# Kernel tuning notes

Hardware: AMD Instinct MI355X
Metric: run time of the kernel (lower is better)

The kernel has to match this reference:

```python
import jax, jax.numpy as jnp
import numpy as np

C = 768
HEADS = 12

def setup_inputs() -> dict:
    key = jax.random.key(0)
    k1, k2, k3 = jax.random.split(key, 3)
    x = jax.random.normal(k1, (8, C, 32, 32), dtype=jnp.float32)
    # 1x1 convs are channel-wise linear maps; store as [out_c, in_c]
    w_qkv = jax.random.normal(k2, (3 * C, C), dtype=jnp.float32) * (C ** -0.5)
    w_proj = jax.random.normal(k3, (C, C), dtype=jnp.float32) * (C ** -0.5)
    return {"x": x, "w_qkv": w_qkv, "w_proj": w_proj}

def reference(x, w_qkv, w_proj):
    b, c, h, w = x.shape
    heads = HEADS
    dh = c // heads
    n = h * w
    scale = dh ** -0.5
    # 1x1 conv QKV: [b, 3c, h, w] -> [b, 3, heads, dh, n]
    qkv = jnp.einsum('oc,bchw->bohw', w_qkv, x).reshape(b, 3, heads, dh, n)
    q, k, v = qkv[:, 0], qkv[:, 1], qkv[:, 2]  # each [b, heads, dh, n]
    attn = jnp.einsum('bhdn,bhdm->bhnm', q, k) * scale  # [b, heads, n, n]
    attn = jax.nn.softmax(attn, axis=-1)
    out = jnp.einsum('bhnm,bhdm->bhdn', attn, v)  # [b, heads, dh, n]
    out = out.reshape(b, c, h, w)
    return jnp.einsum('oc,bchw->bohw', w_proj, out)
```

## Files before the change

### kernel.cpp

```cpp
#include <hip/hip_runtime.h>

typedef unsigned short u16;
typedef unsigned int u32;
typedef float v4f __attribute__((ext_vector_type(4)));
typedef __bf16 bf16x8 __attribute__((ext_vector_type(8)));

#define BATCH 8
#define CDIM 768
#define NHEAD 12
#define DH 64
#define NSEQ 1024
#define SCL 0.18033688011112042f

__device__ __forceinline__ u16 f2bf(float f) {
  u32 u = __builtin_bit_cast(u32, f);
  u += 0x7fffu + ((u >> 16) & 1u);
  return (u16)(u >> 16);
}

__device__ __forceinline__ u16 b16(float f) {
  return (u16)((__builtin_bit_cast(u32, f) + 0x8000u) >> 16);
}

__device__ __forceinline__ u32 pkbf(float hi, float lo) {
  u32 a = __builtin_bit_cast(u32, hi) + 0x8000u;
  u32 b = __builtin_bit_cast(u32, lo) + 0x8000u;
  return __builtin_amdgcn_perm(a, b, 0x07060302u);
}

__device__ __forceinline__ v4f mfma16(bf16x8 a, bf16x8 b, v4f c) {
  return __builtin_amdgcn_mfma_f32_16x16x32_bf16(a, b, c, 0, 0, 0);
}

__device__ __forceinline__ void gload16(const u16* g, u16* l) {
  __builtin_amdgcn_global_load_lds(
      (const __attribute__((address_space(1))) void*)g,
      (__attribute__((address_space(3))) void*)l, 16, 0, 0);
}

__global__ __launch_bounds__(256) void k_prep(const float* __restrict__ x,
                                              const float* __restrict__ wq,
                                              const float* __restrict__ wp,
                                              u16* __restrict__ xT,
                                              u16* __restrict__ wqb,
                                              u16* __restrict__ wpb) {
  __shared__ u16 Ts[64][72];
  int bid = blockIdx.x;
  int t = threadIdx.x;
  if (bid < 2304) {
    bool isQ = bid < 1728;
    const float* s = isQ ? wq : wp;
    u16* d = isQ ? wqb : wpb;
    int i = (isQ ? bid : bid - 1728) * 256 + t;
    float4 v = ((const float4*)s)[i];
    u32 lo = (u32)f2bf(v.x) | ((u32)f2bf(v.y) << 16);
    u32 hi = (u32)f2bf(v.z) | ((u32)f2bf(v.w) << 16);
    ((uint2*)d)[i] = uint2{lo, hi};
    return;
  }
  int id = bid - 2304;
  int p0 = (id & 15) * 64; id >>= 4;
  int c0 = (id % 12) * 64; int b = id / 12;
  int cr = t >> 4;
  int p4 = (t & 15) * 4;
  const float* src = x + ((size_t)b * CDIM + c0) * NSEQ + p0;
#pragma unroll
  for (int i = 0; i < 4; ++i) {
    int c = cr + i * 16;
    float4 v = *(const float4*)&src[(size_t)c * NSEQ + p4];
    Ts[p4 + 0][c] = f2bf(v.x);
    Ts[p4 + 1][c] = f2bf(v.y);
    Ts[p4 + 2][c] = f2bf(v.z);
    Ts[p4 + 3][c] = f2bf(v.w);
  }
  __syncthreads();
  int p = t >> 2;
  int cq = t & 3;
  u16* dst = xT + ((size_t)b * NSEQ + p0 + p) * CDIM + c0;
#pragma unroll
  for (int j = 0; j < 2; ++j) {
    int ch = cq + j * 4;
    *(int4*)&dst[ch * 8] = *(const int4*)&Ts[p][ch * 8];
  }
}

#define NKT 12

__device__ __forceinline__ void gemm_core(const u16* __restrict__ Ag,
                                          const u16* __restrict__ Bg,
                                          u16* sm, v4f (&acc)[4][4]) {
  int t = threadIdx.x, lane = t & 63, wid = t >> 6;
  int ln = lane & 15, quad = lane >> 4;
  int wm = wid >> 2, wn = wid & 3;

  int sr = t >> 3;
  int sc = ((t & 7) ^ (sr & 7)) * 8;
  const u16* As0 = Ag + (size_t)sr * CDIM + sc;
  const u16* Bs0 = Bg + (size_t)sr * CDIM + sc;
  int ldw = wid * 512;

  int x = ln & 7;
  int rA = (wm * 64 + ln) * 64;
  int rB = 8192 + (wn * 64 + ln) * 64;
  int c0 = (quad ^ x) * 8;
  int c1 = ((4 + quad) ^ x) * 8;

  {
    u16* sb = sm;
    gload16(As0, sb + ldw);
    gload16(As0 + (size_t)64 * CDIM, sb + 4096 + ldw);
    gload16(Bs0, sb + 8192 + ldw);
    gload16(Bs0 + (size_t)64 * CDIM, sb + 12288 + ldw);
    gload16(Bs0 + (size_t)128 * CDIM, sb + 16384 + ldw);
    gload16(Bs0 + (size_t)192 * CDIM, sb + 20480 + ldw);
  }
  asm volatile("" ::: "memory");
  {
    u16* sb = sm + 24576;
    const u16* Ak = As0 + 64;
    const u16* Bk = Bs0 + 64;
    gload16(Ak, sb + ldw);
    gload16(Ak + (size_t)64 * CDIM, sb + 4096 + ldw);
    gload16(Bk, sb + 8192 + ldw);
    gload16(Bk + (size_t)64 * CDIM, sb + 12288 + ldw);
    gload16(Bk + (size_t)128 * CDIM, sb + 16384 + ldw);
    gload16(Bk + (size_t)192 * CDIM, sb + 20480 + ldw);
  }
  asm volatile("s_waitcnt vmcnt(6)" ::: "memory");
  asm volatile("s_barrier" ::: "memory");

#pragma unroll
  for (int kt = 0; kt < NKT; ++kt) {
    const u16* sb = sm + (kt % 3) * 24576;
    u16* nb = sm + ((kt + 2) % 3) * 24576;
    const u16* Ak = As0 + (kt + 2) * 64;
    const u16* Bk = Bs0 + (kt + 2) * 64;

    bf16x8 af[2][2], bfr[4][2];
#pragma unroll
    for (int m = 0; m < 2; ++m) {
      af[m][0] = *(const bf16x8*)&sb[rA + m * 1024 + c0];
      af[m][1] = *(const bf16x8*)&sb[rA + m * 1024 + c1];
    }
#pragma unroll
    for (int n = 0; n < 4; ++n) {
      bfr[n][0] = *(const bf16x8*)&sb[rB + n * 1024 + c0];
      bfr[n][1] = *(const bf16x8*)&sb[rB + n * 1024 + c1];
    }
    if (kt < NKT - 2) {
      gload16(Ak, nb + ldw);
      gload16(Ak + (size_t)64 * CDIM, nb + 4096 + ldw);
      gload16(Bk, nb + 8192 + ldw);
    }
    asm volatile("s_barrier" ::: "memory");
    asm volatile("s_waitcnt lgkmcnt(0)" ::: "memory");
    __builtin_amdgcn_sched_barrier(0);
    __builtin_amdgcn_s_setprio(1);
#pragma unroll
    for (int m = 0; m < 2; ++m)
#pragma unroll
      for (int n = 0; n < 4; ++n) {
        acc[m][n] = mfma16(af[m][0], bfr[n][0], acc[m][n]);
        acc[m][n] = mfma16(af[m][1], bfr[n][1], acc[m][n]);
      }
    __builtin_amdgcn_s_setprio(0);
    asm volatile("s_barrier" ::: "memory");

#pragma unroll
    for (int m = 0; m < 2; ++m) {
      af[m][0] = *(const bf16x8*)&sb[rA + (m + 2) * 1024 + c0];
      af[m][1] = *(const bf16x8*)&sb[rA + (m + 2) * 1024 + c1];
    }
    if (kt < NKT - 2) {
      gload16(Bk + (size_t)64 * CDIM, nb + 12288 + ldw);
      gload16(Bk + (size_t)128 * CDIM, nb + 16384 + ldw);
      gload16(Bk + (size_t)192 * CDIM, nb + 20480 + ldw);
      asm volatile("s_waitcnt vmcnt(6)" ::: "memory");
    } else if (kt == NKT - 2) {
      asm volatile("s_waitcnt vmcnt(0)" ::: "memory");
    }
    asm volatile("s_barrier" ::: "memory");
    asm volatile("s_waitcnt lgkmcnt(0)" ::: "memory");
    __builtin_amdgcn_sched_barrier(0);
    __builtin_amdgcn_s_setprio(1);
#pragma unroll
    for (int m = 0; m < 2; ++m)
#pragma unroll
      for (int n = 0; n < 4; ++n) {
        acc[m + 2][n] = mfma16(af[m][0], bfr[n][0], acc[m + 2][n]);
        acc[m + 2][n] = mfma16(af[m][1], bfr[n][1], acc[m + 2][n]);
      }
    __builtin_amdgcn_s_setprio(0);
    asm volatile("s_barrier" ::: "memory");
  }
}

__global__ __launch_bounds__(512, 2) void k_gemm_qkv(const u16* __restrict__ Wb,
                                                     const u16* __restrict__ xT,
                                                     u16* __restrict__ qkT,
                                                     u16* __restrict__ vbuf) {
  __shared__ u16 sm[3 * 24576];
  int bid = blockIdx.x;
  int swz = (bid & 7) * 72 + (bid >> 3);
  int oIdx = swz % 18, pIdx = swz / 18;
  int oT = oIdx * 128;
  int pG = pIdx * 256;

  v4f acc[4][4] = {};
  gemm_core(Wb + (size_t)oT * CDIM, xT + (size_t)pG * CDIM, sm, acc);

  int t = threadIdx.x, lane = t & 63, wid = t >> 6;
  int ln = lane & 15, quad = lane >> 4;
  int wm = wid >> 2, wn = wid & 3;
  bool isV = oT >= 2 * CDIM;
#pragma unroll
  for (int m = 0; m < 4; ++m) {
#pragma unroll
    for (int n = 0; n < 4; ++n) {
      int ro = oT + wm * 64 + m * 16 + quad * 4;
      int cp = pG + wn * 64 + n * 16 + ln;
      int b = cp >> 10, p = cp & 1023;
      if (!isV) {
        u32 lo = (u32)f2bf(acc[m][n][0]) | ((u32)f2bf(acc[m][n][1]) << 16);
        u32 hi = (u32)f2bf(acc[m][n][2]) | ((u32)f2bf(acc[m][n][3]) << 16);
        *(uint2*)&qkT[((size_t)b * NSEQ + p) * 1536 + ro] = uint2{lo, hi};
      } else {
#pragma unroll
        for (int r = 0; r < 4; ++r)
          vbuf[((size_t)b * CDIM + (ro - 2 * CDIM + r)) * NSEQ + p] =
              f2bf(acc[m][n][r]);
      }
    }
  }
}

__global__ __launch_bounds__(256) void k_attn(const u16* __restrict__ qkT,
                                              const u16* __restrict__ vbuf,
                                              u16* __restrict__ attnT) {
  int id = blockIdx.x;
  int b = id & 7;
  int j = id >> 3;
  int h = j % 12;
  int nt0 = (j / 12) * 128;

  int t = threadIdx.x, lane = t & 63, wid = t >> 6;
  int ln = lane & 15, quad = lane >> 4;
  int nbase = nt0 + wid * 32;

  __shared__ u16 Ks[2][2][64 * 32];
  __shared__ u16 Vs[2][2][64 * 32];
  __shared__ u16 Pa[4][32 * 72];
  u16* myP = Pa[wid];

  const u16* qbase = qkT + ((size_t)b * NSEQ + nbase) * 1536 + h * DH;
  bf16x8 aq[2][2];
#pragma unroll
  for (int mt = 0; mt < 2; ++mt)
#pragma unroll
    for (int ks = 0; ks < 2; ++ks)
      aq[mt][ks] = *(const bf16x8*)&qbase[(size_t)(mt * 16 + ln) * 1536 + ks * 32 + quad * 8];

  bf16x8 ones;
#pragma unroll
  for (int i = 0; i < 8; ++i) ones[i] = __builtin_bit_cast(__bf16, (u16)0x3F80);

  v4f oacc[2][4] = {};
  v4f lacc[2] = {};

  int lr = lane >> 2, lc = (lane & 3) * 8;
  const u16* kgw = qkT + (size_t)b * NSEQ * 1536 + CDIM + h * DH +
                   (size_t)(wid * 16 + lr) * 1536 + lc;
  const u16* vgw = vbuf + ((size_t)b * CDIM + h * DH + wid * 16 + lr) * NSEQ + lc;
  int sb = (wid * 16) * 32;

  gload16(kgw, &Ks[0][0][sb]);
  gload16(kgw + 32, &Ks[0][1][sb]);
  gload16(vgw, &Vs[0][0][sb]);
  gload16(vgw + 32, &Vs[0][1][sb]);
  __syncthreads();

  for (int s = 0; s < 16; ++s) {
    int cur = s & 1, nxt = cur ^ 1;
    if (s < 15) {
      size_t ko = (size_t)(s + 1) * 64 * 1536;
      int vo = (s + 1) * 64;
      gload16(kgw + ko, &Ks[nxt][0][sb]);
      gload16(kgw + ko + 32, &Ks[nxt][1][sb]);
      gload16(vgw + vo, &Vs[nxt][0][sb]);
      gload16(vgw + vo + 32, &Vs[nxt][1][sb]);
    }

#pragma unroll
    for (int ct = 0; ct < 4; ++ct) {
      bf16x8 kf0 = *(const bf16x8*)&Ks[cur][0][(ct * 16 + ln) * 32 + quad * 8];
      bf16x8 kf1 = *(const bf16x8*)&Ks[cur][1][(ct * 16 + ln) * 32 + quad * 8];
#pragma unroll
      for (int mt = 0; mt < 2; ++mt) {
        v4f sc = {};
        sc = mfma16(kf0, aq[mt][0], sc);
        sc = mfma16(kf1, aq[mt][1], sc);
        float p0 = __builtin_amdgcn_exp2f(sc[0] * SCL);
        float p1 = __builtin_amdgcn_exp2f(sc[1] * SCL);
        float p2 = __builtin_amdgcn_exp2f(sc[2] * SCL);
        float p3 = __builtin_amdgcn_exp2f(sc[3] * SCL);
        *(uint2*)&myP[(mt * 16 + ln) * 72 + ct * 16 + quad * 4] =
            uint2{pkbf(p1, p0), pkbf(p3, p2)};
      }
    }

    bf16x8 ap[2][2];
#pragma unroll
    for (int mt = 0; mt < 2; ++mt)
#pragma unroll
      for (int ks = 0; ks < 2; ++ks)
        ap[mt][ks] = *(const bf16x8*)&myP[(mt * 16 + ln) * 72 + ks * 32 + quad * 8];
#pragma unroll
    for (int mt = 0; mt < 2; ++mt) {
      lacc[mt] = mfma16(ap[mt][0], ones, lacc[mt]);
      lacc[mt] = mfma16(ap[mt][1], ones, lacc[mt]);
    }
#pragma unroll
    for (int nt = 0; nt < 4; ++nt) {
      bf16x8 vf0 = *(const bf16x8*)&Vs[cur][0][(nt * 16 + ln) * 32 + quad * 8];
      bf16x8 vf1 = *(const bf16x8*)&Vs[cur][1][(nt * 16 + ln) * 32 + quad * 8];
#pragma unroll
      for (int mt = 0; mt < 2; ++mt) {
        oacc[mt][nt] = mfma16(ap[mt][0], vf0, oacc[mt][nt]);
        oacc[mt][nt] = mfma16(ap[mt][1], vf1, oacc[mt][nt]);
      }
    }
    __syncthreads();
  }

#pragma unroll
  for (int mt = 0; mt < 2; ++mt) {
#pragma unroll
    for (int r = 0; r < 4; ++r) {
      float inv = 1.0f / lacc[mt][r];
      int n = nbase + mt * 16 + quad * 4 + r;
      u16* dst = attnT + ((size_t)b * NSEQ + n) * CDIM + h * DH;
#pragma unroll
      for (int nt = 0; nt < 4; ++nt)
        dst[nt * 16 + ln] = b16(oacc[mt][nt][r] * inv);
    }
  }
}

__global__ __launch_bounds__(512, 2) void k_gemm_proj(const u16* __restrict__ Wb,
                                                      const u16* __restrict__ aT,
                                                      float* __restrict__ out) {
  __shared__ u16 sm[3 * 24576];
  int bid = blockIdx.x;
  int swz = (bid & 7) * 24 + (bid >> 3);
  int oIdx = swz % 6, pIdx = swz / 6;
  int oT = oIdx * 128;
  int pG = pIdx * 256;

  v4f acc[4][4] = {};
  gemm_core(Wb + (size_t)oT * CDIM, aT + (size_t)pG * CDIM, sm, acc);

  int t = threadIdx.x, lane = t & 63, wid = t >> 6;
  int ln = lane & 15, quad = lane >> 4;
  int wm = wid >> 2, wn = wid & 3;
#pragma unroll
  for (int m = 0; m < 4; ++m) {
#pragma unroll
    for (int n = 0; n < 4; ++n) {
      int ro = oT + wm * 64 + m * 16 + quad * 4;
      int cp = pG + wn * 64 + n * 16 + ln;
      int b = cp >> 10, p = cp & 1023;
#pragma unroll
      for (int r = 0; r < 4; ++r)
        out[((size_t)b * CDIM + ro + r) * NSEQ + p] = acc[m][n][r];
    }
  }
}

extern "C" void kernel_launch(void* const* d_in, const int* in_sizes, int n_in,
                              void* d_out, int out_size, void* d_ws, size_t ws_size,
                              hipStream_t stream) {
  const float* x = (const float*)d_in[0];
  const float* w_qkv = (const float*)d_in[1];
  const float* w_proj = (const float*)d_in[2];
  float* out = (float*)d_out;

  char* ws = (char*)d_ws;
  u16* wqkv_bf = (u16*)(ws);
  u16* wproj_bf = (u16*)(ws + 3538944);
  u16* xT = (u16*)(ws + 4718592);
  u16* vbuf = (u16*)(ws + 17301504);
  u16* qkT = (u16*)d_out;
  u16* attnT = xT;

  k_prep<<<dim3(3840), dim3(256), 0, stream>>>(x, w_qkv, w_proj, xT, wqkv_bf, wproj_bf);
  k_gemm_qkv<<<dim3(576), dim3(512), 0, stream>>>(wqkv_bf, xT, qkT, vbuf);
  k_attn<<<dim3(768), dim3(256), 0, stream>>>(qkT, vbuf, attnT);
  k_gemm_proj<<<dim3(192), dim3(512), 0, stream>>>(wproj_bf, attnT, out);
}
```

Measured before the change: 190.8 us.

## Retile GEMMs to 256x128 with 4 waves and k=32 steps; swizzle attention K/V LDS

The shared GEMM core moves from 8 waves with a 128x256 tile and K-step 64 to 4 waves with a 256x128 tile, K-step 32, and a 3-stage ring unrolled by three. Each wave now holds 8x4 accumulators and a new XOR swizzle for LDS. The aim is more MFMA work per wave and less LDS traffic per FLOP, at the cost of more register pressure and twice as many barriers per K. The attention kernel separately switches its K/V tiles to 64-wide rows with an XOR swizzle to cut LDS bank conflicts.

After: 184.6 us. -3.3%, faster.

```diff
diff --git a/kernel.cpp b/kernel.cpp
--- a/kernel.cpp
+++ b/kernel.cpp
@@ -84,140 +84,128 @@
   }
 }
 
-#define NKT 12
+#define NKT 24
 
 __device__ __forceinline__ void gemm_core(const u16* __restrict__ Ag,
                                           const u16* __restrict__ Bg,
-                                          u16* sm, v4f (&acc)[4][4]) {
+                                          u16* sm, v4f (&acc)[8][4]) {
   int t = threadIdx.x, lane = t & 63, wid = t >> 6;
   int ln = lane & 15, quad = lane >> 4;
-  int wm = wid >> 2, wn = wid & 3;
-
-  int sr = t >> 3;
-  int sc = ((t & 7) ^ (sr & 7)) * 8;
-  const u16* As0 = Ag + (size_t)sr * CDIM + sc;
-  const u16* Bs0 = Bg + (size_t)sr * CDIM + sc;
+  int wm = wid >> 1, wn = wid & 1;
+
+  int srow = wid * 16 + (lane >> 2);
+  int scg = ((lane & 3) ^ ((lane >> 3) & 3)) * 8;
+  const u16* As0 = Ag + (size_t)srow * CDIM + scg;
+  const u16* Bs0 = Bg + (size_t)srow * CDIM + scg;
   int ldw = wid * 512;
 
-  int x = ln & 7;
-  int rA = (wm * 64 + ln) * 64;
-  int rB = 8192 + (wn * 64 + ln) * 64;
-  int c0 = (quad ^ x) * 8;
-  int c1 = ((4 + quad) ^ x) * 8;
+  int cA = (quad ^ ((ln >> 1) & 3)) * 8;
+  int rA = (wm * 128 + ln) * 32;
+  int rB = 8192 + (wn * 64 + ln) * 32;
 
   {
-    u16* sb = sm;
-    gload16(As0, sb + ldw);
-    gload16(As0 + (size_t)64 * CDIM, sb + 4096 + ldw);
-    gload16(Bs0, sb + 8192 + ldw);
-    gload16(Bs0 + (size_t)64 * CDIM, sb + 12288 + ldw);
-    gload16(Bs0 + (size_t)128 * CDIM, sb + 16384 + ldw);
-    gload16(Bs0 + (size_t)192 * CDIM, sb + 20480 + ldw);
+    u16* sb0 = sm;
+    gload16(As0, sb0 + ldw);
+    gload16(As0 + (size_t)64 * CDIM, sb0 + 2048 + ldw);
+    gload16(As0 + (size_t)128 * CDIM, sb0 + 4096 + ldw);
+    gload16(As0 + (size_t)192 * CDIM, sb0 + 6144 + ldw);
+    gload16(Bs0, sb0 + 8192 + ldw);
+    gload16(Bs0 + (size_t)64 * CDIM, sb0 + 10240 + ldw);
   }
   asm volatile("" ::: "memory");
   {
-    u16* sb = sm + 24576;
-    const u16* Ak = As0 + 64;
-    const u16* Bk = Bs0 + 64;
-    gload16(Ak, sb + ldw);
-    gload16(Ak + (size_t)64 * CDIM, sb + 4096 + ldw);
-    gload16(Bk, sb + 8192 + ldw);
-    gload16(Bk + (size_t)64 * CDIM, sb + 12288 + ldw);
-    gload16(Bk + (size_t)128 * CDIM, sb + 16384 + ldw);
-    gload16(Bk + (size_t)192 * CDIM, sb + 20480 + ldw);
+    u16* sb1 = sm + 12288;
+    gload16(As0 + 32, sb1 + ldw);
+    gload16(As0 + (size_t)64 * CDIM + 32, sb1 + 2048 + ldw);
+    gload16(As0 + (size_t)128 * CDIM + 32, sb1 + 4096 + ldw);
+    gload16(As0 + (size_t)192 * CDIM + 32, sb1 + 6144 + ldw);
+    gload16(Bs0 + 32, sb1 + 8192 + ldw);
+    gload16(Bs0 + (size_t)64 * CDIM + 32, sb1 + 10240 + ldw);
   }
   asm volatile("s_waitcnt vmcnt(6)" ::: "memory");
   asm volatile("s_barrier" ::: "memory");
 
-#pragma unroll
-  for (int kt = 0; kt < NKT; ++kt) {
-    const u16* sb = sm + (kt % 3) * 24576;
-    u16* nb = sm + ((kt + 2) % 3) * 24576;
-    const u16* Ak = As0 + (kt + 2) * 64;
-    const u16* Bk = Bs0 + (kt + 2) * 64;
-
-    bf16x8 af[2][2], bfr[4][2];
-#pragma unroll
-    for (int m = 0; m < 2; ++m) {
-      af[m][0] = *(const bf16x8*)&sb[rA + m * 1024 + c0];
-      af[m][1] = *(const bf16x8*)&sb[rA + m * 1024 + c1];
-    }
-#pragma unroll
-    for (int n = 0; n < 4; ++n) {
-      bfr[n][0] = *(const bf16x8*)&sb[rB + n * 1024 + c0];
-      bfr[n][1] = *(const bf16x8*)&sb[rB + n * 1024 + c1];
-    }
-    if (kt < NKT - 2) {
-      gload16(Ak, nb + ldw);
-      gload16(Ak + (size_t)64 * CDIM, nb + 4096 + ldw);
-      gload16(Bk, nb + 8192 + ldw);
-    }
-    asm volatile("s_barrier" ::: "memory");
-    asm volatile("s_waitcnt lgkmcnt(0)" ::: "memory");
-    __builtin_amdgcn_sched_barrier(0);
-    __builtin_amdgcn_s_setprio(1);
-#pragma unroll
-    for (int m = 0; m < 2; ++m)
-#pragma unroll
-      for (int n = 0; n < 4; ++n) {
-        acc[m][n] = mfma16(af[m][0], bfr[n][0], acc[m][n]);
-        acc[m][n] = mfma16(af[m][1], bfr[n][1], acc[m][n]);
-      }
-    __builtin_amdgcn_s_setprio(0);
-    asm volatile("s_barrier" ::: "memory");
-
-#pragma unroll
-    for (int m = 0; m < 2; ++m) {
-      af[m][0] = *(const bf16x8*)&sb[rA + (m + 2) * 1024 + c0];
-      af[m][1] = *(const bf16x8*)&sb[rA + (m + 2) * 1024 + c1];
-    }
-    if (kt < NKT - 2) {
-      gload16(Bk + (size_t)64 * CDIM, nb + 12288 + ldw);
-      gload16(Bk + (size_t)128 * CDIM, nb + 16384 + ldw);
-      gload16(Bk + (size_t)192 * CDIM, nb + 20480 + ldw);
-      asm volatile("s_waitcnt vmcnt(6)" ::: "memory");
-    } else if (kt == NKT - 2) {
-      asm volatile("s_waitcnt vmcnt(0)" ::: "memory");
-    }
-    asm volatile("s_barrier" ::: "memory");
-    asm volatile("s_waitcnt lgkmcnt(0)" ::: "memory");
-    __builtin_amdgcn_sched_barrier(0);
-    __builtin_amdgcn_s_setprio(1);
-#pragma unroll
-    for (int m = 0; m < 2; ++m)
-#pragma unroll
-      for (int n = 0; n < 4; ++n) {
-        acc[m + 2][n] = mfma16(af[m][0], bfr[n][0], acc[m + 2][n]);
-        acc[m + 2][n] = mfma16(af[m][1], bfr[n][1], acc[m + 2][n]);
-      }
-    __builtin_amdgcn_s_setprio(0);
-    asm volatile("s_barrier" ::: "memory");
-  }
-}
-
-__global__ __launch_bounds__(512, 2) void k_gemm_qkv(const u16* __restrict__ Wb,
+  for (int kb = 0; kb < 8; ++kb) {
+#pragma unroll
+    for (int u = 0; u < 3; ++u) {
+      int kt = kb * 3 + u;
+      const u16* sb = sm + u * 12288;
+      u16* nb = sm + ((u + 2) % 3) * 12288;
+      int ko = (kt + 2) * 32;
+
+      bf16x8 af[4], bfr[4];
+#pragma unroll
+      for (int m = 0; m < 4; ++m)
+        af[m] = *(const bf16x8*)&sb[rA + m * 512 + cA];
+#pragma unroll
+      for (int n = 0; n < 4; ++n)
+        bfr[n] = *(const bf16x8*)&sb[rB + n * 512 + cA];
+      if (kt < NKT - 2) {
+        gload16(As0 + ko, nb + ldw);
+        gload16(As0 + (size_t)64 * CDIM + ko, nb + 2048 + ldw);
+        gload16(Bs0 + ko, nb + 8192 + ldw);
+      }
+      asm volatile("s_barrier" ::: "memory");
+      asm volatile("s_waitcnt lgkmcnt(0)" ::: "memory");
+      __builtin_amdgcn_sched_barrier(0);
+      __builtin_amdgcn_s_setprio(1);
+#pragma unroll
+      for (int m = 0; m < 4; ++m)
+#pragma unroll
+        for (int n = 0; n < 4; ++n)
+          acc[m][n] = mfma16(af[m], bfr[n], acc[m][n]);
+      __builtin_amdgcn_s_setprio(0);
+      asm volatile("s_barrier" ::: "memory");
+
+#pragma unroll
+      for (int m = 0; m < 4; ++m)
+        af[m] = *(const bf16x8*)&sb[rA + (m + 4) * 512 + cA];
+      if (kt < NKT - 2) {
+        gload16(As0 + (size_t)128 * CDIM + ko, nb + 4096 + ldw);
+        gload16(As0 + (size_t)192 * CDIM + ko, nb + 6144 + ldw);
+        gload16(Bs0 + (size_t)64 * CDIM + ko, nb + 10240 + ldw);
+        asm volatile("s_waitcnt vmcnt(6)" ::: "memory");
+      } else if (kt == NKT - 2) {
+        asm volatile("s_waitcnt vmcnt(0)" ::: "memory");
+      }
+      asm volatile("s_barrier" ::: "memory");
+      asm volatile("s_waitcnt lgkmcnt(0)" ::: "memory");
+      __builtin_amdgcn_sched_barrier(0);
+      __builtin_amdgcn_s_setprio(1);
+#pragma unroll
+      for (int m = 0; m < 4; ++m)
+#pragma unroll
+        for (int n = 0; n < 4; ++n)
+          acc[m + 4][n] = mfma16(af[m], bfr[n], acc[m + 4][n]);
+      __builtin_amdgcn_s_setprio(0);
+      asm volatile("s_barrier" ::: "memory");
+    }
+  }
+}
+
+__global__ __launch_bounds__(256, 2) void k_gemm_qkv(const u16* __restrict__ Wb,
                                                      const u16* __restrict__ xT,
                                                      u16* __restrict__ qkT,
                                                      u16* __restrict__ vbuf) {
-  __shared__ u16 sm[3 * 24576];
+  __shared__ u16 sm[3 * 12288];
   int bid = blockIdx.x;
   int swz = (bid & 7) * 72 + (bid >> 3);
-  int oIdx = swz % 18, pIdx = swz / 18;
-  int oT = oIdx * 128;
-  int pG = pIdx * 256;
-
-  v4f acc[4][4] = {};
+  int oIdx = swz % 9, pIdx = swz / 9;
+  int oT = oIdx * 256;
+  int pG = pIdx * 128;
+
+  v4f acc[8][4] = {};
   gemm_core(Wb + (size_t)oT * CDIM, xT + (size_t)pG * CDIM, sm, acc);
 
   int t = threadIdx.x, lane = t & 63, wid = t >> 6;
   int ln = lane & 15, quad = lane >> 4;
-  int wm = wid >> 2, wn = wid & 3;
+  int wm = wid >> 1, wn = wid & 1;
   bool isV = oT >= 2 * CDIM;
 #pragma unroll
-  for (int m = 0; m < 4; ++m) {
+  for (int m = 0; m < 8; ++m) {
 #pragma unroll
     for (int n = 0; n < 4; ++n) {
-      int ro = oT + wm * 64 + m * 16 + quad * 4;
+      int ro = oT + wm * 128 + m * 16 + quad * 4;
       int cp = pG + wn * 64 + n * 16 + ln;
       int b = cp >> 10, p = cp & 1023;
       if (!isV) {
@@ -247,8 +235,8 @@
   int ln = lane & 15, quad = lane >> 4;
   int nbase = nt0 + wid * 32;
 
-  __shared__ u16 Ks[2][2][64 * 32];
-  __shared__ u16 Vs[2][2][64 * 32];
+  __shared__ u16 Ks[2][64 * 64];
+  __shared__ u16 Vs[2][64 * 64];
   __shared__ u16 Pa[4][32 * 72];
   u16* myP = Pa[wid];
 
@@ -267,16 +255,19 @@
   v4f oacc[2][4] = {};
   v4f lacc[2] = {};
 
-  int lr = lane >> 2, lc = (lane & 3) * 8;
-  const u16* kgw = qkT + (size_t)b * NSEQ * 1536 + CDIM + h * DH +
-                   (size_t)(wid * 16 + lr) * 1536 + lc;
-  const u16* vgw = vbuf + ((size_t)b * CDIM + h * DH + wid * 16 + lr) * NSEQ + lc;
-  int sb = (wid * 16) * 32;
-
-  gload16(kgw, &Ks[0][0][sb]);
-  gload16(kgw + 32, &Ks[0][1][sb]);
-  gload16(vgw, &Vs[0][0][sb]);
-  gload16(vgw + 32, &Vs[0][1][sb]);
+  int sr8 = lane >> 3;
+  int sch = ((lane & 7) ^ sr8) * 8;
+  const u16* kg0 = qkT + ((size_t)b * NSEQ + wid * 16 + sr8) * 1536 + CDIM + h * DH + sch;
+  const u16* vg0 = vbuf + ((size_t)b * CDIM + h * DH + wid * 16 + sr8) * NSEQ + sch;
+  int sK = (wid * 16) * 64;
+
+  int sw0 = (quad ^ (ln & 7)) * 8;
+  int sw1 = ((4 + quad) ^ (ln & 7)) * 8;
+
+  gload16(kg0, &Ks[0][sK]);
+  gload16(kg0 + (size_t)8 * 1536, &Ks[0][sK + 512]);
+  gload16(vg0, &Vs[0][sK]);
+  gload16(vg0 + 8 * NSEQ, &Vs[0][sK + 512]);
   __syncthreads();
 
   for (int s = 0; s < 16; ++s) {
@@ -284,16 +275,16 @@
     if (s < 15) {
       size_t ko = (size_t)(s + 1) * 64 * 1536;
       int vo = (s + 1) * 64;
-      gload16(kgw + ko, &Ks[nxt][0][sb]);
-      gload16(kgw + ko + 32, &Ks[nxt][1][sb]);
-      gload16(vgw + vo, &Vs[nxt][0][sb]);
-      gload16(vgw + vo + 32, &Vs[nxt][1][sb]);
+      gload16(kg0 + ko, &Ks[nxt][sK]);
+      gload16(kg0 + ko + (size_t)8 * 1536, &Ks[nxt][sK + 512]);
+      gload16(vg0 + vo, &Vs[nxt][sK]);
+      gload16(vg0 + vo + 8 * NSEQ, &Vs[nxt][sK + 512]);
     }
 
 #pragma unroll
     for (int ct = 0; ct < 4; ++ct) {
-      bf16x8 kf0 = *(const bf16x8*)&Ks[cur][0][(ct * 16 + ln) * 32 + quad * 8];
-      bf16x8 kf1 = *(const bf16x8*)&Ks[cur][1][(ct * 16 + ln) * 32 + quad * 8];
+      bf16x8 kf0 = *(const bf16x8*)&Ks[cur][(ct * 16 + ln) * 64 + sw0];
+      bf16x8 kf1 = *(const bf16x8*)&Ks[cur][(ct * 16 + ln) * 64 + sw1];
 #pragma unroll
       for (int mt = 0; mt < 2; ++mt) {
         v4f sc = {};
@@ -321,8 +312,8 @@
     }
 #pragma unroll
     for (int nt = 0; nt < 4; ++nt) {
-      bf16x8 vf0 = *(const bf16x8*)&Vs[cur][0][(nt * 16 + ln) * 32 + quad * 8];
-      bf16x8 vf1 = *(const bf16x8*)&Vs[cur][1][(nt * 16 + ln) * 32 + quad * 8];
+      bf16x8 vf0 = *(const bf16x8*)&Vs[cur][(nt * 16 + ln) * 64 + sw0];
+      bf16x8 vf1 = *(const bf16x8*)&Vs[cur][(nt * 16 + ln) * 64 + sw1];
 #pragma unroll
       for (int mt = 0; mt < 2; ++mt) {
         oacc[mt][nt] = mfma16(ap[mt][0], vf0, oacc[mt][nt]);
@@ -346,27 +337,27 @@
   }
 }
 
-__global__ __launch_bounds__(512, 2) void k_gemm_proj(const u16* __restrict__ Wb,
+__global__ __launch_bounds__(256, 2) void k_gemm_proj(const u16* __restrict__ Wb,
                                                       const u16* __restrict__ aT,
                                                       float* __restrict__ out) {
-  __shared__ u16 sm[3 * 24576];
+  __shared__ u16 sm[3 * 12288];
   int bid = blockIdx.x;
   int swz = (bid & 7) * 24 + (bid >> 3);
-  int oIdx = swz % 6, pIdx = swz / 6;
-  int oT = oIdx * 128;
-  int pG = pIdx * 256;
-
-  v4f acc[4][4] = {};
+  int oIdx = swz % 3, pIdx = swz / 3;
+  int oT = oIdx * 256;
+  int pG = pIdx * 128;
+
+  v4f acc[8][4] = {};
   gemm_core(Wb + (size_t)oT * CDIM, aT + (size_t)pG * CDIM, sm, acc);
 
   int t = threadIdx.x, lane = t & 63, wid = t >> 6;
   int ln = lane & 15, quad = lane >> 4;
-  int wm = wid >> 2, wn = wid & 3;
-#pragma unroll
-  for (int m = 0; m < 4; ++m) {
+  int wm = wid >> 1, wn = wid & 1;
+#pragma unroll
+  for (int m = 0; m < 8; ++m) {
 #pragma unroll
     for (int n = 0; n < 4; ++n) {
-      int ro = oT + wm * 64 + m * 16 + quad * 4;
+      int ro = oT + wm * 128 + m * 16 + quad * 4;
       int cp = pG + wn * 64 + n * 16 + ln;
       int b = cp >> 10, p = cp & 1023;
 #pragma unroll
@@ -393,7 +384,7 @@
   u16* attnT = xT;
 
   k_prep<<<dim3(3840), dim3(256), 0, stream>>>(x, w_qkv, w_proj, xT, wqkv_bf, wproj_bf);
-  k_gemm_qkv<<<dim3(576), dim3(512), 0, stream>>>(wqkv_bf, xT, qkT, vbuf);
+  k_gemm_qkv<<<dim3(576), dim3(256), 0, stream>>>(wqkv_bf, xT, qkT, vbuf);
   k_attn<<<dim3(768), dim3(256), 0, stream>>>(qkT, vbuf, attnT);
-  k_gemm_proj<<<dim3(192), dim3(512), 0, stream>>>(wproj_bf, attnT, out);
-}
+  k_gemm_proj<<<dim3(192), dim3(256), 0, stream>>>(wproj_bf, attnT, out);
+}
```
